# Performance work log

Measured on AMD Instinct MI355X. Metric: run time of the kernel, lower is better.

The kernel has to match this reference:

```python
import jax, jax.numpy as jnp
import numpy as np

NPOINT = 1024
RADIUS = 0.2
NSAMPLE = 32
EPS = 1e-5


def farthest_point_sample(xyz, npoint):
    # xyz: [B, N, 3] -> [B, npoint] int32, deterministic start at index 0
    B, N, _ = xyz.shape

    def step(carry, _):
        dist, farthest = carry
        centroid = jnp.take_along_axis(xyz, farthest[:, None, None], axis=1)  # [B,1,3]
        d = jnp.sum((xyz - centroid) ** 2, axis=-1)  # [B,N]
        dist = jnp.minimum(dist, d)
        nxt = jnp.argmax(dist, axis=-1).astype(jnp.int32)
        return (dist, nxt), farthest

    init = (jnp.full((B, N), 1e10, dtype=xyz.dtype), jnp.zeros((B,), dtype=jnp.int32))
    _, idxs = jax.lax.scan(step, init, None, length=npoint)
    return idxs.T  # [B, npoint]


def query_ball_point(radius, nsample, xyz, new_xyz):
    # xyz: [B,N,3], new_xyz: [B,S,3] -> [B,S,nsample] int32
    N = xyz.shape[1]
    sqr = jnp.sum((new_xyz[:, :, None, :] - xyz[:, None, :, :]) ** 2, axis=-1)  # [B,S,N]
    ar = jnp.arange(N, dtype=jnp.int32)
    gidx = jnp.where(sqr > radius ** 2, N, ar[None, None, :])
    gidx = jnp.sort(gidx, axis=-1)[:, :, :nsample]  # sorts index values, matching torch
    first = gidx[:, :, :1]
    return jnp.where(gidx == N, first, gidx)


def mlp_layer(h, w, b, g, be, m, v):
    # h: [B, Cin, K, S]; 1x1 Conv2d + BatchNorm2d(eval) + ReLU
    h = jnp.einsum('oc,bcks->boks', w, h) + b[None, :, None, None]
    h = (h - m[None, :, None, None]) * (g[None, :, None, None] / jnp.sqrt(v[None, :, None, None] + EPS)) + be[None, :, None, None]
    return jax.nn.relu(h)


def setup_inputs() -> dict:
    key = jax.random.key(0)
    ks = jax.random.split(key, 24)
    inp = {
        'xyz': jax.random.normal(ks[0], (1, 16, 3, 4096), jnp.float32),
        'points': jax.random.normal(ks[1], (1, 16, 64, 4096), jnp.float32),
        'w0': jax.random.normal(ks[2], (64, 67), jnp.float32) * 0.1,
        'b0': jax.random.normal(ks[3], (64,), jnp.float32) * 0.1,
        'g0': jax.random.uniform(ks[4], (64,), jnp.float32),
        'be0': jax.random.normal(ks[5], (64,), jnp.float32) * 0.1,
        'm0': jax.random.normal(ks[6], (64,), jnp.float32) * 0.1,
        'v0': jax.random.uniform(ks[7], (64,), jnp.float32),
        'w1': jax.random.normal(ks[8], (64, 64), jnp.float32) * 0.1,
        'b1': jax.random.normal(ks[9], (64,), jnp.float32) * 0.1,
        'g1': jax.random.uniform(ks[10], (64,), jnp.float32),
        'be1': jax.random.normal(ks[11], (64,), jnp.float32) * 0.1,
        'm1': jax.random.normal(ks[12], (64,), jnp.float32) * 0.1,
        'v1': jax.random.uniform(ks[13], (64,), jnp.float32),
        'w2': jax.random.normal(ks[14], (128, 64), jnp.float32) * 0.1,
        'b2': jax.random.normal(ks[15], (128,), jnp.float32) * 0.1,
        'g2': jax.random.uniform(ks[16], (128,), jnp.float32),
        'be2': jax.random.normal(ks[17], (128,), jnp.float32) * 0.1,
        'm2': jax.random.normal(ks[18], (128,), jnp.float32) * 0.1,
        'v2': jax.random.uniform(ks[19], (128,), jnp.float32),
    }
    return inp


def reference(xyz, points, w0, b0, g0, be0, m0, v0, w1, b1, g1, be1, m1, v1, w2, b2, g2, be2, m2, v2):
    T, B, C, N = xyz.shape
    BT = T * B
    x = xyz.reshape(BT, C, N).transpose(0, 2, 1)          # [B', N, 3]
    p = points.reshape(BT, -1, N).transpose(0, 2, 1)      # [B', N, D]

    fps_idx = farthest_point_sample(x, NPOINT)            # [B', S]
    bidx = jnp.arange(BT)[:, None]
    new_xyz = x[bidx, fps_idx]                            # [B', S, 3]

    idx = query_ball_point(RADIUS, NSAMPLE, x, new_xyz)   # [B', S, K]
    b3 = jnp.arange(BT)[:, None, None]
    grouped_xyz = x[b3, idx]                              # [B', S, K, 3]
    grouped_norm = grouped_xyz - new_xyz[:, :, None, :]
    grouped_p = p[b3, idx]                                # [B', S, K, D]
    new_points = jnp.concatenate([grouped_norm, grouped_p], axis=-1)  # [B', S, K, 3+D]

    h = new_points.transpose(0, 3, 2, 1)                  # [B', 3+D, K, S]
    h = mlp_layer(h, w0, b0, g0, be0, m0, v0)
    h = mlp_layer(h, w1, b1, g1, be1, m1, v1)
    h = mlp_layer(h, w2, b2, g2, be2, m2, v2)
    out = jnp.max(h, axis=2)                              # [B', Cout, S]

    new_xyz_out = new_xyz.transpose(0, 2, 1).reshape(T, B, C, NPOINT)
    return new_xyz_out, out
```

## Files before the change

### kernel.cpp

```cpp
#include <hip/hip_runtime.h>
#include <hip/hip_bf16.h>

#define NPTS    4096
#define NBATCH  16
#define NPOINT  1024
#define NSAMPLE 32

#define ROW_SHR1  0x111
#define ROW_SHR2  0x112
#define ROW_SHR4  0x114
#define ROW_SHR8  0x118
#define ROW_BC15  0x142
#define ROW_BC31  0x143

template<int CTRL>
__device__ __forceinline__ unsigned dpp_mov(unsigned v) {
    return (unsigned)__builtin_amdgcn_update_dpp(0, (int)v, CTRL, 0xF, 0xF, true);
}
template<int CTRL>
__device__ __forceinline__ unsigned long long dpp_max64(unsigned long long k) {
    unsigned lo = dpp_mov<CTRL>((unsigned)(k & 0xFFFFFFFFull));
    unsigned hi = dpp_mov<CTRL>((unsigned)(k >> 32));
    unsigned long long t = ((unsigned long long)hi << 32) | (unsigned long long)lo;
    return (t > k) ? t : k;
}
template<int CTRL>
__device__ __forceinline__ float dpp_maxf(float v) {
    unsigned t = dpp_mov<CTRL>(__float_as_uint(v));
    return fmaxf(v, __uint_as_float(t));
}

__global__ __launch_bounds__(256) void fps_kernel(
    const float* __restrict__ xyz, float* __restrict__ newxyz)
{
    const int b    = blockIdx.x;
    const int tid  = threadIdx.x;
    const int lane = tid & 63;
    const int w    = tid >> 6;
    const float* xb = xyz + (size_t)b * 3 * NPTS;

    __shared__ float4 P[NPTS];
    __shared__ unsigned long long slots[2][4];

    float px[16], py[16], pz[16], dist[16];
    #pragma unroll
    for (int q = 0; q < 4; ++q) {
        const int n4 = tid * 16 + q * 4;
        float4 xs = *(const float4*)(xb + n4);
        float4 ys = *(const float4*)(xb + NPTS + n4);
        float4 zs = *(const float4*)(xb + 2*NPTS + n4);
        px[q*4+0] = xs.x; px[q*4+1] = xs.y; px[q*4+2] = xs.z; px[q*4+3] = xs.w;
        py[q*4+0] = ys.x; py[q*4+1] = ys.y; py[q*4+2] = ys.z; py[q*4+3] = ys.w;
        pz[q*4+0] = zs.x; pz[q*4+1] = zs.y; pz[q*4+2] = zs.z; pz[q*4+3] = zs.w;
        P[n4+0] = make_float4(xs.x, ys.x, zs.x, 0.f);
        P[n4+1] = make_float4(xs.y, ys.y, zs.y, 0.f);
        P[n4+2] = make_float4(xs.z, ys.z, zs.z, 0.f);
        P[n4+3] = make_float4(xs.w, ys.w, zs.w, 0.f);
    }
    #pragma unroll
    for (int j = 0; j < 16; ++j) dist[j] = 1e10f;
    __syncthreads();

    float4 c0 = P[0];
    float cx = c0.x, cy = c0.y, cz = c0.z;
    if (tid == 0) {
        newxyz[b*3*NPOINT + 0]        = cx;
        newxyz[b*3*NPOINT + NPOINT]   = cy;
        newxyz[b*3*NPOINT + 2*NPOINT] = cz;
    }

    for (int i = 1; i < NPOINT; ++i) {
        float bv = -1.0f; int bj = 0;
        #pragma unroll
        for (int j = 0; j < 16; ++j) {
            float dx = px[j] - cx;
            float dy = py[j] - cy;
            float dz = pz[j] - cz;
            float d = __fadd_rn(__fadd_rn(__fmul_rn(dx,dx), __fmul_rn(dy,dy)),
                                __fmul_rn(dz,dz));
            float nd = fminf(dist[j], d);
            dist[j] = nd;
            if (nd > bv) { bv = nd; bj = j; }
        }
        const int myidx = (tid << 4) | bj;

        float wv = bv;
        wv = dpp_maxf<ROW_SHR1>(wv);
        wv = dpp_maxf<ROW_SHR2>(wv);
        wv = dpp_maxf<ROW_SHR4>(wv);
        wv = dpp_maxf<ROW_SHR8>(wv);
        wv = dpp_maxf<ROW_BC15>(wv);
        wv = dpp_maxf<ROW_BC31>(wv);
        float wmax = __uint_as_float(
            (unsigned)__builtin_amdgcn_readlane((int)__float_as_uint(wv), 63));
        unsigned long long mask = __ballot(bv == wmax);
        int L = (int)__builtin_ctzll(mask);
        int widx = __builtin_amdgcn_readlane(myidx, L);

        if (lane == 0)
            slots[i & 1][w] =
                ((unsigned long long)__float_as_uint(wmax) << 32) |
                (unsigned long long)(unsigned)(~widx);
        __syncthreads();

        unsigned long long kk = slots[i & 1][lane & 3];
        kk = dpp_max64<ROW_SHR1>(kk);
        kk = dpp_max64<ROW_SHR2>(kk);
        unsigned flo = (unsigned)__builtin_amdgcn_readlane(
            (int)(unsigned)(kk & 0xFFFFFFFFull), 3);
        const int f = (int)(~flo);

        float4 cc = P[f];
        cx = cc.x; cy = cc.y; cz = cc.z;
        if (tid == 0) {
            newxyz[b*3*NPOINT + i]            = cx;
            newxyz[b*3*NPOINT + NPOINT + i]   = cy;
            newxyz[b*3*NPOINT + 2*NPOINT + i] = cz;
        }
    }
}

__global__ __launch_bounds__(256) void ball_kernel(
    const float* __restrict__ xyz, const float* __restrict__ newxyz,
    int* __restrict__ ball_idx)
{
    const int gid  = blockIdx.x * 256 + threadIdx.x;
    const int wid  = gid >> 6;
    const int lane = threadIdx.x & 63;
    const int b    = wid >> 10;
    const int m    = wid & (NPOINT - 1);
    const float r2 = (float)(0.2 * 0.2);

    const float* xb = xyz + (size_t)b * 3 * NPTS;
    const float cx = newxyz[b*3*NPOINT + m];
    const float cy = newxyz[b*3*NPOINT + NPOINT + m];
    const float cz = newxyz[b*3*NPOINT + 2*NPOINT + m];
    int* out = ball_idx + (size_t)wid * NSAMPLE;

    int base = 0, first = 0;
    for (int c0 = 0; c0 < NPTS; c0 += 64) {
        const int n = c0 + lane;
        float dx = xb[n] - cx, dy = xb[NPTS+n] - cy, dz = xb[2*NPTS+n] - cz;
        float d = __fadd_rn(__fadd_rn(__fmul_rn(dx,dx), __fmul_rn(dy,dy)),
                            __fmul_rn(dz,dz));
        bool inb = (d <= r2);
        unsigned long long mask = __ballot(inb);
        if (base == 0 && mask != 0ull) first = c0 + (int)__builtin_ctzll(mask);
        int pos = base + __popcll(mask & ((1ull << lane) - 1ull));
        if (inb && pos < NSAMPLE) out[pos] = n;
        base += __popcll(mask);
        if (base >= NSAMPLE) break;
    }
    if (lane < NSAMPLE && lane >= base) out[lane] = first;
}

__global__ __launch_bounds__(256) void setup_kernel(
    const float* __restrict__ w0, const float* __restrict__ b0,
    const float* __restrict__ g0, const float* __restrict__ be0,
    const float* __restrict__ m0, const float* __restrict__ v0,
    const float* __restrict__ w1, const float* __restrict__ b1,
    const float* __restrict__ g1, const float* __restrict__ be1,
    const float* __restrict__ m1, const float* __restrict__ v1,
    const float* __restrict__ b2, const float* __restrict__ g2,
    const float* __restrict__ be2, const float* __restrict__ m2,
    const float* __restrict__ v2, float* __restrict__ wp)
{
    const int t = threadIdx.x;
    for (int i = t; i < 64*67; i += 256) {
        int o = i / 67, k = i - o*67;
        wp[k*64 + o] = w0[i];
    }
    for (int i = t; i < 64*64; i += 256) {
        int o = i >> 6, k = i & 63;
        wp[4288 + k*64 + o] = w1[i];
    }
    if (t < 64) {
        float s0 = g0[t] / sqrtf(v0[t] + 1e-5f);
        wp[8384 + t] = s0;
        wp[8448 + t] = (b0[t] - m0[t]) * s0 + be0[t];
        float s1 = g1[t] / sqrtf(v1[t] + 1e-5f);
        wp[8512 + t] = s1;
        wp[8576 + t] = (b1[t] - m1[t]) * s1 + be1[t];
    }
    if (t < 128) {
        float s2 = g2[t] / sqrtf(v2[t] + 1e-5f);
        wp[8640 + t] = s2;
        wp[8768 + t] = (b2[t] - m2[t]) * s2 + be2[t];
    }
}

__global__ __launch_bounds__(256) void mlp_kernel(
    const float* __restrict__ xyz, const float* __restrict__ points,
    const float* __restrict__ newxyz, const int* __restrict__ ball_idx,
    const float* __restrict__ wp, const float* __restrict__ w2,
    float* __restrict__ out)
{
    const int col = blockIdx.x * 256 + threadIdx.x;
    const int m   = (col >> 5) & (NPOINT - 1);
    const int b   = col >> 15;
    const int p   = ball_idx[col];

    const float* xb = xyz + (size_t)b * 3 * NPTS;
    float in[67];
    in[0] = xb[p]          - newxyz[b*3*NPOINT + m];
    in[1] = xb[NPTS + p]   - newxyz[b*3*NPOINT + NPOINT + m];
    in[2] = xb[2*NPTS + p] - newxyz[b*3*NPOINT + 2*NPOINT + m];
    const float* pb = points + (size_t)b * 64 * NPTS;
    #pragma unroll
    for (int c = 0; c < 64; ++c) in[3 + c] = pb[c * NPTS + p];

    const float* w0t = wp;
    const float* w1t = wp + 4288;
    const float* sc0 = wp + 8384;
    const float* sh0 = wp + 8448;
    const float* sc1 = wp + 8512;
    const float* sh1 = wp + 8576;
    const float* sc2 = wp + 8640;
    const float* sh2 = wp + 8768;

    float h[64];
    #pragma unroll
    for (int o = 0; o < 64; ++o) h[o] = 0.0f;
    #pragma unroll
    for (int k = 0; k < 67; ++k) {
        const float x = in[k];
        #pragma unroll
        for (int o = 0; o < 64; ++o) h[o] = fmaf(w0t[k*64 + o], x, h[o]);
    }
    #pragma unroll
    for (int o = 0; o < 64; ++o)
        h[o] = fmaxf(fmaf(h[o], sc0[o], sh0[o]), 0.0f);

    float g[64];
    #pragma unroll
    for (int o = 0; o < 64; ++o) g[o] = 0.0f;
    #pragma unroll
    for (int k = 0; k < 64; ++k) {
        const float x = h[k];
        #pragma unroll
        for (int o = 0; o < 64; ++o) g[o] = fmaf(w1t[k*64 + o], x, g[o]);
    }
    #pragma unroll
    for (int o = 0; o < 64; ++o)
        g[o] = fmaxf(fmaf(g[o], sc1[o], sh1[o]), 0.0f);

    float* outb = out + (size_t)b * 128 * NPOINT + m;
    #pragma unroll 2
    for (int o = 0; o < 128; ++o) {
        float acc = 0.0f;
        const float* wr = w2 + o * 64;
        #pragma unroll
        for (int k = 0; k < 64; ++k) acc = fmaf(wr[k], g[k], acc);
        acc = fmaxf(fmaf(acc, sc2[o], sh2[o]), 0.0f);
        acc = dpp_maxf<ROW_SHR1>(acc);
        acc = dpp_maxf<ROW_SHR2>(acc);
        acc = dpp_maxf<ROW_SHR4>(acc);
        acc = dpp_maxf<ROW_SHR8>(acc);
        acc = dpp_maxf<ROW_BC15>(acc);
        if ((threadIdx.x & 31) == 31) outb[o * NPOINT] = acc;
    }
}

extern "C" void kernel_launch(void* const* d_in, const int* in_sizes, int n_in,
                              void* d_out, int out_size, void* d_ws, size_t ws_size,
                              hipStream_t stream)
{
    const float* xyz    = (const float*)d_in[0];
    const float* points = (const float*)d_in[1];
    const float* w0  = (const float*)d_in[2];
    const float* b0  = (const float*)d_in[3];
    const float* g0  = (const float*)d_in[4];
    const float* be0 = (const float*)d_in[5];
    const float* m0  = (const float*)d_in[6];
    const float* v0  = (const float*)d_in[7];
    const float* w1  = (const float*)d_in[8];
    const float* b1  = (const float*)d_in[9];
    const float* g1  = (const float*)d_in[10];
    const float* be1 = (const float*)d_in[11];
    const float* m1  = (const float*)d_in[12];
    const float* v1  = (const float*)d_in[13];
    const float* w2  = (const float*)d_in[14];
    const float* b2  = (const float*)d_in[15];
    const float* g2  = (const float*)d_in[16];
    const float* be2 = (const float*)d_in[17];
    const float* m2  = (const float*)d_in[18];
    const float* v2  = (const float*)d_in[19];

    float* out0 = (float*)d_out;
    float* out1 = out0 + NBATCH * 3 * NPOINT;

    int*   ball = (int*)d_ws;
    float* wp   = (float*)((char*)d_ws + (size_t)NBATCH*NPOINT*NSAMPLE*sizeof(int));

    hipLaunchKernelGGL(setup_kernel, dim3(1), dim3(256), 0, stream,
                       w0,b0,g0,be0,m0,v0, w1,b1,g1,be1,m1,v1, b2,g2,be2,m2,v2, wp);
    hipLaunchKernelGGL(fps_kernel,  dim3(NBATCH), dim3(256), 0, stream, xyz, out0);
    hipLaunchKernelGGL(ball_kernel, dim3(NBATCH*NPOINT/4), dim3(256), 0, stream,
                       xyz, out0, ball);
    hipLaunchKernelGGL(mlp_kernel,  dim3(NBATCH*NPOINT*NSAMPLE/256), dim3(256), 0, stream,
                       xyz, points, out0, ball, wp, w2, out1);
}
```

Before: 1.106 ms.

## Shorten FPS critical path by carrying winner coordinates and using 512 threads

```diff
diff --git a/kernel.cpp b/kernel.cpp
--- a/kernel.cpp
+++ b/kernel.cpp
@@ -18,19 +18,16 @@
     return (unsigned)__builtin_amdgcn_update_dpp(0, (int)v, CTRL, 0xF, 0xF, true);
 }
 template<int CTRL>
-__device__ __forceinline__ unsigned long long dpp_max64(unsigned long long k) {
-    unsigned lo = dpp_mov<CTRL>((unsigned)(k & 0xFFFFFFFFull));
-    unsigned hi = dpp_mov<CTRL>((unsigned)(k >> 32));
-    unsigned long long t = ((unsigned long long)hi << 32) | (unsigned long long)lo;
-    return (t > k) ? t : k;
-}
-template<int CTRL>
 __device__ __forceinline__ float dpp_maxf(float v) {
     unsigned t = dpp_mov<CTRL>(__float_as_uint(v));
     return fmaxf(v, __uint_as_float(t));
 }
-
-__global__ __launch_bounds__(256) void fps_kernel(
+__device__ __forceinline__ float readlane_f(float v, int lane) {
+    return __uint_as_float(
+        (unsigned)__builtin_amdgcn_readlane((int)__float_as_uint(v), lane));
+}
+
+__global__ __launch_bounds__(512) void fps_kernel(
     const float* __restrict__ xyz, float* __restrict__ newxyz)
 {
     const int b    = blockIdx.x;
@@ -39,40 +36,30 @@
     const int w    = tid >> 6;
     const float* xb = xyz + (size_t)b * 3 * NPTS;
 
-    __shared__ float4 P[NPTS];
-    __shared__ unsigned long long slots[2][4];
-
-    float px[16], py[16], pz[16], dist[16];
-    #pragma unroll
-    for (int q = 0; q < 4; ++q) {
-        const int n4 = tid * 16 + q * 4;
+    __shared__ float4 slots[2][8];
+    __shared__ float NX[NPOINT], NY[NPOINT], NZ[NPOINT];
+
+    float px[8], py[8], pz[8], dist[8];
+    #pragma unroll
+    for (int q = 0; q < 2; ++q) {
+        const int n4 = tid * 8 + q * 4;
         float4 xs = *(const float4*)(xb + n4);
         float4 ys = *(const float4*)(xb + NPTS + n4);
         float4 zs = *(const float4*)(xb + 2*NPTS + n4);
         px[q*4+0] = xs.x; px[q*4+1] = xs.y; px[q*4+2] = xs.z; px[q*4+3] = xs.w;
         py[q*4+0] = ys.x; py[q*4+1] = ys.y; py[q*4+2] = ys.z; py[q*4+3] = ys.w;
         pz[q*4+0] = zs.x; pz[q*4+1] = zs.y; pz[q*4+2] = zs.z; pz[q*4+3] = zs.w;
-        P[n4+0] = make_float4(xs.x, ys.x, zs.x, 0.f);
-        P[n4+1] = make_float4(xs.y, ys.y, zs.y, 0.f);
-        P[n4+2] = make_float4(xs.z, ys.z, zs.z, 0.f);
-        P[n4+3] = make_float4(xs.w, ys.w, zs.w, 0.f);
-    }
-    #pragma unroll
-    for (int j = 0; j < 16; ++j) dist[j] = 1e10f;
-    __syncthreads();
-
-    float4 c0 = P[0];
-    float cx = c0.x, cy = c0.y, cz = c0.z;
-    if (tid == 0) {
-        newxyz[b*3*NPOINT + 0]        = cx;
-        newxyz[b*3*NPOINT + NPOINT]   = cy;
-        newxyz[b*3*NPOINT + 2*NPOINT] = cz;
-    }
+    }
+    #pragma unroll
+    for (int j = 0; j < 8; ++j) dist[j] = 1e10f;
+
+    float cx = xb[0], cy = xb[NPTS], cz = xb[2*NPTS];
+    if (tid == 0) { NX[0] = cx; NY[0] = cy; NZ[0] = cz; }
 
     for (int i = 1; i < NPOINT; ++i) {
-        float bv = -1.0f; int bj = 0;
-        #pragma unroll
-        for (int j = 0; j < 16; ++j) {
+        float bv = -1.0f, bx = 0.f, by = 0.f, bz = 0.f;
+        #pragma unroll
+        for (int j = 0; j < 8; ++j) {
             float dx = px[j] - cx;
             float dy = py[j] - cy;
             float dz = pz[j] - cz;
@@ -80,9 +67,12 @@
                                 __fmul_rn(dz,dz));
             float nd = fminf(dist[j], d);
             dist[j] = nd;
-            if (nd > bv) { bv = nd; bj = j; }
+            bool t = nd > bv;
+            bv = t ? nd    : bv;
+            bx = t ? px[j] : bx;
+            by = t ? py[j] : by;
+            bz = t ? pz[j] : bz;
         }
-        const int myidx = (tid << 4) | bj;
 
         float wv = bv;
         wv = dpp_maxf<ROW_SHR1>(wv);
@@ -91,32 +81,35 @@
         wv = dpp_maxf<ROW_SHR8>(wv);
         wv = dpp_maxf<ROW_BC15>(wv);
         wv = dpp_maxf<ROW_BC31>(wv);
-        float wmax = __uint_as_float(
-            (unsigned)__builtin_amdgcn_readlane((int)__float_as_uint(wv), 63));
+        float wmax = readlane_f(wv, 63);
         unsigned long long mask = __ballot(bv == wmax);
         int L = (int)__builtin_ctzll(mask);
-        int widx = __builtin_amdgcn_readlane(myidx, L);
-
+        float sx = readlane_f(bx, L);
+        float sy = readlane_f(by, L);
+        float sz = readlane_f(bz, L);
         if (lane == 0)
-            slots[i & 1][w] =
-                ((unsigned long long)__float_as_uint(wmax) << 32) |
-                (unsigned long long)(unsigned)(~widx);
+            slots[i & 1][w] = make_float4(wmax, sx, sy, sz);
         __syncthreads();
 
-        unsigned long long kk = slots[i & 1][lane & 3];
-        kk = dpp_max64<ROW_SHR1>(kk);
-        kk = dpp_max64<ROW_SHR2>(kk);
-        unsigned flo = (unsigned)__builtin_amdgcn_readlane(
-            (int)(unsigned)(kk & 0xFFFFFFFFull), 3);
-        const int f = (int)(~flo);
-
-        float4 cc = P[f];
-        cx = cc.x; cy = cc.y; cz = cc.z;
-        if (tid == 0) {
-            newxyz[b*3*NPOINT + i]            = cx;
-            newxyz[b*3*NPOINT + NPOINT + i]   = cy;
-            newxyz[b*3*NPOINT + 2*NPOINT + i] = cz;
-        }
+        float4 s = slots[i & 1][lane & 7];
+        float v = s.x;
+        v = dpp_maxf<ROW_SHR1>(v);
+        v = dpp_maxf<ROW_SHR2>(v);
+        v = dpp_maxf<ROW_SHR4>(v);
+        float gmax = readlane_f(v, 7);
+        unsigned long long m2 = __ballot(s.x == gmax);
+        int W = (int)__builtin_ctzll(m2);
+        cx = readlane_f(s.y, W);
+        cy = readlane_f(s.z, W);
+        cz = readlane_f(s.w, W);
+        if (tid == 0) { NX[i] = cx; NY[i] = cy; NZ[i] = cz; }
+    }
+
+    __syncthreads();
+    for (int t = tid; t < NPOINT; t += 512) {
+        newxyz[b*3*NPOINT + t]            = NX[t];
+        newxyz[b*3*NPOINT + NPOINT + t]   = NY[t];
+        newxyz[b*3*NPOINT + 2*NPOINT + t] = NZ[t];
     }
 }
 
@@ -294,7 +287,7 @@
 
     hipLaunchKernelGGL(setup_kernel, dim3(1), dim3(256), 0, stream,
                        w0,b0,g0,be0,m0,v0, w1,b1,g1,be1,m1,v1, b2,g2,be2,m2,v2, wp);
-    hipLaunchKernelGGL(fps_kernel,  dim3(NBATCH), dim3(256), 0, stream, xyz, out0);
+    hipLaunchKernelGGL(fps_kernel,  dim3(NBATCH), dim3(512), 0, stream, xyz, out0);
     hipLaunchKernelGGL(ball_kernel, dim3(NBATCH*NPOINT/4), dim3(256), 0, stream,
                        xyz, out0, ball);
     hipLaunchKernelGGL(mlp_kernel,  dim3(NBATCH*NPOINT*NSAMPLE/256), dim3(256), 0, stream,
```

Result: slower. 1.265 ms (+14.4%).
